# Kernel optimization log

Measured on AMD Instinct MI355X. Metric: run time of the kernel, lower is better.

Reference implementation:

```python
import jax, jax.numpy as jnp
import numpy as np
from jax import lax

CROP = 4
DATA_RANGE = 255.0
KSIZE = 11


def _box_filter(x):
    # x: [B,1,H,W]; 11x11 uniform kernel, padding 5 (SAME), single channel
    k = jnp.ones((1, 1, KSIZE, KSIZE), dtype=x.dtype) / (KSIZE * KSIZE)
    return lax.conv_general_dilated(
        x, k, window_strides=(1, 1), padding=[(5, 5), (5, 5)],
        dimension_numbers=("NCHW", "OIHW", "NCHW"))


def setup_inputs() -> dict:
    key = jax.random.key(0)
    k1, k2 = jax.random.split(key)
    img1 = jax.random.uniform(k1, (16, 3, 512, 512), dtype=jnp.float32) * DATA_RANGE
    img2 = jax.random.uniform(k2, (16, 3, 512, 512), dtype=jnp.float32) * DATA_RANGE
    return {"img1": img1, "img2": img2}


def reference(img1, img2):
    # only_test_y_channel: take channel 0
    x1 = img1[:, 0:1, :, :]
    x2 = img2[:, 0:1, :, :]
    # crop_border = 4
    x1 = x1[:, :, CROP:-CROP, CROP:-CROP].astype(jnp.float32)
    x2 = x2[:, :, CROP:-CROP, CROP:-CROP].astype(jnp.float32)

    C1 = (0.01 * DATA_RANGE) ** 2
    C2 = (0.03 * DATA_RANGE) ** 2

    mu1 = _box_filter(x1)
    mu2 = _box_filter(x2)
    mu1_sq = mu1 * mu1
    mu2_sq = mu2 * mu2
    mu1_mu2 = mu1 * mu2
    sigma1_sq = _box_filter(x1 * x1) - mu1_sq
    sigma2_sq = _box_filter(x2 * x2) - mu2_sq
    sigma12 = _box_filter(x1 * x2) - mu1_mu2

    ssim_map = ((2 * mu1_mu2 + C1) * (2 * sigma12 + C2)) / (
        (mu1_sq + mu2_sq + C1) * (sigma1_sq + sigma2_sq + C2))
    return jnp.mean(ssim_map)
```

## Files before the change

### kernel.cpp

```cpp
#include <hip/hip_runtime.h>

#define CROPPX 4
#define H 504
#define W 504
#define IMG 512
#define NB 16
#define NCH 3
#define KS 11
#define RAD 5
#define TW 64
#define STRIP (TW + 2*RAD)
#define RPS 28
#define NSEG 18
#define NXT 8
#define TOTAL (RPS + 2*RAD)

__global__ __launch_bounds__(64) void ssim_main(const float* __restrict__ img1,
                                                const float* __restrict__ img2,
                                                float* __restrict__ partial) {
    const int tid = threadIdx.x;
    const int gx0 = blockIdx.x * TW;
    const int y0  = blockIdx.y * RPS;
    const int b   = blockIdx.z;

    __shared__ float2 rowAB[STRIP];

    const float* p1 = img1 + (size_t)(b * NCH) * IMG * IMG + (size_t)CROPPX * IMG + CROPPX;
    const float* p2 = img2 + (size_t)(b * NCH) * IMG * IMG + (size_t)CROPPX * IMG + CROPPX;

    float r1[KS], r2[KS], r11[KS], r22[KS], r12[KS];
    #pragma unroll
    for (int j = 0; j < KS; ++j) { r1[j]=0.f; r2[j]=0.f; r11[j]=0.f; r22[j]=0.f; r12[j]=0.f; }

    float vs1 = 0.f, vs2 = 0.f, vs11 = 0.f, vs22 = 0.f, vs12 = 0.f;
    float ssum = 0.f;
    const float C1 = 6.5025f, C2 = 58.5225f;
    const float inv121 = 1.0f / 121.0f;
    const bool colValid = (gx0 + tid) < W;
    const int c0 = gx0 - RAD + tid;
    const int c1 = c0 + 64;
    const bool lane2 = tid < (STRIP - 64);

    float a0 = 0.f, b0 = 0.f, a1 = 0.f, b1 = 0.f;
    {
        const int r = y0 - RAD;
        if ((unsigned)r < (unsigned)H) {
            const size_t ro = (size_t)r * IMG;
            if ((unsigned)c0 < (unsigned)W) { a0 = p1[ro + c0]; b0 = p2[ro + c0]; }
            if (lane2 && (unsigned)c1 < (unsigned)W) { a1 = p1[ro + c1]; b1 = p2[ro + c1]; }
        }
    }

    for (int base = 0; base < TOTAL; base += KS) {
        #pragma unroll
        for (int j = 0; j < KS; ++j) {
            const int iter = base + j;
            if (iter >= TOTAL) break;

            __syncthreads();
            rowAB[tid] = make_float2(a0, b0);
            if (lane2) rowAB[64 + tid] = make_float2(a1, b1);
            __syncthreads();

            a0 = 0.f; b0 = 0.f; a1 = 0.f; b1 = 0.f;
            if (iter + 1 < TOTAL) {
                const int rn = y0 - RAD + iter + 1;
                if ((unsigned)rn < (unsigned)H) {
                    const size_t ro = (size_t)rn * IMG;
                    if ((unsigned)c0 < (unsigned)W) { a0 = p1[ro + c0]; b0 = p2[ro + c0]; }
                    if (lane2 && (unsigned)c1 < (unsigned)W) { a1 = p1[ro + c1]; b1 = p2[ro + c1]; }
                }
            }

            float h1 = 0.f, h2 = 0.f, h11 = 0.f, h22 = 0.f, h12 = 0.f;
            #pragma unroll
            for (int dx = 0; dx < KS; ++dx) {
                const float2 ab = rowAB[tid + dx];
                h1 += ab.x;
                h2 += ab.y;
                h11 = fmaf(ab.x, ab.x, h11);
                h22 = fmaf(ab.y, ab.y, h22);
                h12 = fmaf(ab.x, ab.y, h12);
            }

            vs1  += h1  - r1[j];  r1[j]  = h1;
            vs2  += h2  - r2[j];  r2[j]  = h2;
            vs11 += h11 - r11[j]; r11[j] = h11;
            vs22 += h22 - r22[j]; r22[j] = h22;
            vs12 += h12 - r12[j]; r12[j] = h12;

            if (iter >= 2 * RAD && colValid) {
                const float mu1 = vs1 * inv121;
                const float mu2 = vs2 * inv121;
                const float mu1s = mu1 * mu1;
                const float mu2s = mu2 * mu2;
                const float m12  = mu1 * mu2;
                const float s1  = fmaf(vs11, inv121, -mu1s);
                const float s2  = fmaf(vs22, inv121, -mu2s);
                const float s12 = fmaf(vs12, inv121, -m12);
                const float num = (2.0f * m12 + C1) * (2.0f * s12 + C2);
                const float den = (mu1s + mu2s + C1) * (s1 + s2 + C2);
                ssum += num / den;
            }
        }
    }

    for (int off = 32; off > 0; off >>= 1)
        ssum += __shfl_down(ssum, off);
    if (tid == 0) {
        const int bidx = (blockIdx.z * gridDim.y + blockIdx.y) * gridDim.x + blockIdx.x;
        partial[bidx] = ssum;
    }
}

__global__ __launch_bounds__(256) void ssim_final(const float* __restrict__ partial,
                                                  int n, float* __restrict__ out) {
    __shared__ double sh[256];
    double s = 0.0;
    for (int i = threadIdx.x; i < n; i += 256) s += (double)partial[i];
    sh[threadIdx.x] = s;
    __syncthreads();
    for (int stride = 128; stride > 0; stride >>= 1) {
        if (threadIdx.x < stride) sh[threadIdx.x] += sh[threadIdx.x + stride];
        __syncthreads();
    }
    if (threadIdx.x == 0)
        out[0] = (float)(sh[0] / ((double)NB * (double)H * (double)W));
}

extern "C" void kernel_launch(void* const* d_in, const int* in_sizes, int n_in,
                              void* d_out, int out_size, void* d_ws, size_t ws_size,
                              hipStream_t stream) {
    const float* img1 = (const float*)d_in[0];
    const float* img2 = (const float*)d_in[1];
    float* out = (float*)d_out;
    float* partial = (float*)d_ws;

    dim3 grid(NXT, NSEG, NB);
    ssim_main<<<grid, 64, 0, stream>>>(img1, img2, partial);
    ssim_final<<<1, 256, 0, stream>>>(partial, NXT * NSEG * NB, out);
}
```

Measured before the change: 132.1 us.

## Preload whole row strip into shared memory before filtering, drop per-row barriers

Instead of streaming one row at a time through a shared buffer with two barriers per row and a one-row prefetch, each block now loads its full 28-row strip into shared memory up front in batches of 7 rows (many loads in flight), syncs once, then runs the sliding-window filter. The strip height drops to 18 rows with more segments, giving more blocks but more halo overhead (28 rows loaded for 18 outputs). The division is also replaced with a fast hardware reciprocal, which slightly loosens precision.

```diff
diff --git a/kernel.cpp b/kernel.cpp
--- a/kernel.cpp
+++ b/kernel.cpp
@@ -10,10 +10,11 @@
 #define RAD 5
 #define TW 64
 #define STRIP (TW + 2*RAD)
-#define RPS 28
-#define NSEG 18
+#define RPS 18
+#define NSEG 28
 #define NXT 8
-#define TOTAL (RPS + 2*RAD)
+#define ROWS (RPS + 2*RAD)
+#define CHUNK 7
 
 __global__ __launch_bounds__(64) void ssim_main(const float* __restrict__ img1,
                                                 const float* __restrict__ img2,
@@ -23,10 +24,38 @@
     const int y0  = blockIdx.y * RPS;
     const int b   = blockIdx.z;
 
-    __shared__ float2 rowAB[STRIP];
+    __shared__ float2 strip[ROWS][STRIP];
 
     const float* p1 = img1 + (size_t)(b * NCH) * IMG * IMG + (size_t)CROPPX * IMG + CROPPX;
     const float* p2 = img2 + (size_t)(b * NCH) * IMG * IMG + (size_t)CROPPX * IMG + CROPPX;
+
+    const int c0 = gx0 - RAD + tid;
+    const int c1 = c0 + 64;
+    const bool lane2 = tid < (STRIP - 64);
+    const bool c0ok = (unsigned)c0 < (unsigned)W;
+    const bool c1ok = lane2 && ((unsigned)c1 < (unsigned)W);
+
+    #pragma unroll
+    for (int rc = 0; rc < ROWS / CHUNK; ++rc) {
+        float a0[CHUNK], b0[CHUNK], a1[CHUNK], b1[CHUNK];
+        #pragma unroll
+        for (int j = 0; j < CHUNK; ++j) {
+            const int r = y0 - RAD + rc * CHUNK + j;
+            a0[j] = 0.f; b0[j] = 0.f; a1[j] = 0.f; b1[j] = 0.f;
+            if ((unsigned)r < (unsigned)H) {
+                const size_t ro = (size_t)r * IMG;
+                if (c0ok) { a0[j] = p1[ro + c0]; b0[j] = p2[ro + c0]; }
+                if (c1ok) { a1[j] = p1[ro + c1]; b1[j] = p2[ro + c1]; }
+            }
+        }
+        #pragma unroll
+        for (int j = 0; j < CHUNK; ++j) {
+            const int r = rc * CHUNK + j;
+            strip[r][tid] = make_float2(a0[j], b0[j]);
+            if (lane2) strip[r][64 + tid] = make_float2(a1[j], b1[j]);
+        }
+    }
+    __syncthreads();
 
     float r1[KS], r2[KS], r11[KS], r22[KS], r12[KS];
     #pragma unroll
@@ -37,45 +66,17 @@
     const float C1 = 6.5025f, C2 = 58.5225f;
     const float inv121 = 1.0f / 121.0f;
     const bool colValid = (gx0 + tid) < W;
-    const int c0 = gx0 - RAD + tid;
-    const int c1 = c0 + 64;
-    const bool lane2 = tid < (STRIP - 64);
 
-    float a0 = 0.f, b0 = 0.f, a1 = 0.f, b1 = 0.f;
-    {
-        const int r = y0 - RAD;
-        if ((unsigned)r < (unsigned)H) {
-            const size_t ro = (size_t)r * IMG;
-            if ((unsigned)c0 < (unsigned)W) { a0 = p1[ro + c0]; b0 = p2[ro + c0]; }
-            if (lane2 && (unsigned)c1 < (unsigned)W) { a1 = p1[ro + c1]; b1 = p2[ro + c1]; }
-        }
-    }
-
-    for (int base = 0; base < TOTAL; base += KS) {
+    for (int base = 0; base < ROWS; base += KS) {
         #pragma unroll
         for (int j = 0; j < KS; ++j) {
             const int iter = base + j;
-            if (iter >= TOTAL) break;
-
-            __syncthreads();
-            rowAB[tid] = make_float2(a0, b0);
-            if (lane2) rowAB[64 + tid] = make_float2(a1, b1);
-            __syncthreads();
-
-            a0 = 0.f; b0 = 0.f; a1 = 0.f; b1 = 0.f;
-            if (iter + 1 < TOTAL) {
-                const int rn = y0 - RAD + iter + 1;
-                if ((unsigned)rn < (unsigned)H) {
-                    const size_t ro = (size_t)rn * IMG;
-                    if ((unsigned)c0 < (unsigned)W) { a0 = p1[ro + c0]; b0 = p2[ro + c0]; }
-                    if (lane2 && (unsigned)c1 < (unsigned)W) { a1 = p1[ro + c1]; b1 = p2[ro + c1]; }
-                }
-            }
+            if (iter >= ROWS) break;
 
             float h1 = 0.f, h2 = 0.f, h11 = 0.f, h22 = 0.f, h12 = 0.f;
             #pragma unroll
             for (int dx = 0; dx < KS; ++dx) {
-                const float2 ab = rowAB[tid + dx];
+                const float2 ab = strip[iter][tid + dx];
                 h1 += ab.x;
                 h2 += ab.y;
                 h11 = fmaf(ab.x, ab.x, h11);
@@ -100,7 +101,7 @@
                 const float s12 = fmaf(vs12, inv121, -m12);
                 const float num = (2.0f * m12 + C1) * (2.0f * s12 + C2);
                 const float den = (mu1s + mu2s + C1) * (s1 + s2 + C2);
-                ssum += num / den;
+                ssum = fmaf(num, __builtin_amdgcn_rcpf(den), ssum);
             }
         }
     }
```

Measured after the change: 143.7 us. +8.8%, slower.

## Pack four independent row-strip wavefronts per block and drop block barriers

Applied to the files above, without the earlier changes.

Each 256-thread block now runs four wavefronts, each with its own private shared-memory row buffer and its own 21-row strip. Because a row buffer is only touched by one wave, the two __syncthreads per row are removed. Loads now use clamped addresses with select-based zeroing instead of branches, and the per-pixel division becomes a hardware reciprocal plus FMA. Shorter strips mean a larger share of the 10 halo rows is recomputed per output row, and the approximate reciprocal may change rounding slightly.

```diff
diff --git a/kernel.cpp b/kernel.cpp
--- a/kernel.cpp
+++ b/kernel.cpp
@@ -10,23 +10,35 @@
 #define RAD 5
 #define TW 64
 #define STRIP (TW + 2*RAD)
-#define RPS 28
-#define NSEG 18
+#define RPS 21
+#define WPB 4
+#define BROWS (RPS * WPB)
+#define NYB 6
 #define NXT 8
 #define TOTAL (RPS + 2*RAD)
 
-__global__ __launch_bounds__(64) void ssim_main(const float* __restrict__ img1,
-                                                const float* __restrict__ img2,
-                                                float* __restrict__ partial) {
-    const int tid = threadIdx.x;
-    const int gx0 = blockIdx.x * TW;
-    const int y0  = blockIdx.y * RPS;
-    const int b   = blockIdx.z;
+__global__ __launch_bounds__(256, 4) void ssim_main(const float* __restrict__ img1,
+                                                    const float* __restrict__ img2,
+                                                    float* __restrict__ partial) {
+    const int lane = threadIdx.x & 63;
+    const int wv   = threadIdx.x >> 6;
+    const int gx0  = blockIdx.x * TW;
+    const int y0   = blockIdx.y * BROWS + wv * RPS;
+    const int b    = blockIdx.z;
 
-    __shared__ float2 rowAB[STRIP];
+    __shared__ float2 rowBuf[WPB][STRIP];
+    float2* const myRow = rowBuf[wv];
 
     const float* p1 = img1 + (size_t)(b * NCH) * IMG * IMG + (size_t)CROPPX * IMG + CROPPX;
     const float* p2 = img2 + (size_t)(b * NCH) * IMG * IMG + (size_t)CROPPX * IMG + CROPPX;
+
+    const int  c0   = gx0 - RAD + lane;
+    const int  c0c  = min(max(c0, 0), W - 1);
+    const bool c0ok = (unsigned)c0 < (unsigned)W;
+    const int  c1   = c0 + 64;
+    const int  c1c  = min(c1, W - 1);
+    const bool c1ok = (unsigned)c1 < (unsigned)W;
+    const bool lane2 = lane < (STRIP - 64);
 
     float r1[KS], r2[KS], r11[KS], r22[KS], r12[KS];
     #pragma unroll
@@ -36,18 +48,21 @@
     float ssum = 0.f;
     const float C1 = 6.5025f, C2 = 58.5225f;
     const float inv121 = 1.0f / 121.0f;
-    const bool colValid = (gx0 + tid) < W;
-    const int c0 = gx0 - RAD + tid;
-    const int c1 = c0 + 64;
-    const bool lane2 = tid < (STRIP - 64);
+    const bool colValid = (gx0 + lane) < W;
 
-    float a0 = 0.f, b0 = 0.f, a1 = 0.f, b1 = 0.f;
+    float a0, b0, a1 = 0.f, b1 = 0.f;
     {
-        const int r = y0 - RAD;
-        if ((unsigned)r < (unsigned)H) {
-            const size_t ro = (size_t)r * IMG;
-            if ((unsigned)c0 < (unsigned)W) { a0 = p1[ro + c0]; b0 = p2[ro + c0]; }
-            if (lane2 && (unsigned)c1 < (unsigned)W) { a1 = p1[ro + c1]; b1 = p2[ro + c1]; }
+        const int r  = y0 - RAD;
+        const int rc = min(max(r, 0), H - 1);
+        const bool rok = (unsigned)r < (unsigned)H;
+        const size_t ro = (size_t)rc * IMG;
+        const float ta0 = p1[ro + c0c], tb0 = p2[ro + c0c];
+        a0 = (rok && c0ok) ? ta0 : 0.f;
+        b0 = (rok && c0ok) ? tb0 : 0.f;
+        if (lane2) {
+            const float ta1 = p1[ro + c1c], tb1 = p2[ro + c1c];
+            a1 = (rok && c1ok) ? ta1 : 0.f;
+            b1 = (rok && c1ok) ? tb1 : 0.f;
         }
     }
 
@@ -57,25 +72,28 @@
             const int iter = base + j;
             if (iter >= TOTAL) break;
 
-            __syncthreads();
-            rowAB[tid] = make_float2(a0, b0);
-            if (lane2) rowAB[64 + tid] = make_float2(a1, b1);
-            __syncthreads();
+            myRow[lane] = make_float2(a0, b0);
+            if (lane2) myRow[64 + lane] = make_float2(a1, b1);
 
-            a0 = 0.f; b0 = 0.f; a1 = 0.f; b1 = 0.f;
             if (iter + 1 < TOTAL) {
-                const int rn = y0 - RAD + iter + 1;
-                if ((unsigned)rn < (unsigned)H) {
-                    const size_t ro = (size_t)rn * IMG;
-                    if ((unsigned)c0 < (unsigned)W) { a0 = p1[ro + c0]; b0 = p2[ro + c0]; }
-                    if (lane2 && (unsigned)c1 < (unsigned)W) { a1 = p1[ro + c1]; b1 = p2[ro + c1]; }
+                const int r  = y0 - RAD + iter + 1;
+                const int rc = min(max(r, 0), H - 1);
+                const bool rok = (unsigned)r < (unsigned)H;
+                const size_t ro = (size_t)rc * IMG;
+                const float ta0 = p1[ro + c0c], tb0 = p2[ro + c0c];
+                a0 = (rok && c0ok) ? ta0 : 0.f;
+                b0 = (rok && c0ok) ? tb0 : 0.f;
+                if (lane2) {
+                    const float ta1 = p1[ro + c1c], tb1 = p2[ro + c1c];
+                    a1 = (rok && c1ok) ? ta1 : 0.f;
+                    b1 = (rok && c1ok) ? tb1 : 0.f;
                 }
             }
 
             float h1 = 0.f, h2 = 0.f, h11 = 0.f, h22 = 0.f, h12 = 0.f;
             #pragma unroll
             for (int dx = 0; dx < KS; ++dx) {
-                const float2 ab = rowAB[tid + dx];
+                const float2 ab = myRow[lane + dx];
                 h1 += ab.x;
                 h2 += ab.y;
                 h11 = fmaf(ab.x, ab.x, h11);
@@ -100,15 +118,15 @@
                 const float s12 = fmaf(vs12, inv121, -m12);
                 const float num = (2.0f * m12 + C1) * (2.0f * s12 + C2);
                 const float den = (mu1s + mu2s + C1) * (s1 + s2 + C2);
-                ssum += num / den;
+                ssum = fmaf(num, __builtin_amdgcn_rcpf(den), ssum);
             }
         }
     }
 
     for (int off = 32; off > 0; off >>= 1)
         ssum += __shfl_down(ssum, off);
-    if (tid == 0) {
-        const int bidx = (blockIdx.z * gridDim.y + blockIdx.y) * gridDim.x + blockIdx.x;
+    if (lane == 0) {
+        const int bidx = (((blockIdx.z * gridDim.y + blockIdx.y) * gridDim.x + blockIdx.x) * WPB) + wv;
         partial[bidx] = ssum;
     }
 }
@@ -136,7 +154,7 @@
     float* out = (float*)d_out;
     float* partial = (float*)d_ws;
 
-    dim3 grid(NXT, NSEG, NB);
-    ssim_main<<<grid, 64, 0, stream>>>(img1, img2, partial);
-    ssim_final<<<1, 256, 0, stream>>>(partial, NXT * NSEG * NB, out);
+    dim3 grid(NXT, NYB, NB);
+    ssim_main<<<grid, 256, 0, stream>>>(img1, img2, partial);
+    ssim_final<<<1, 256, 0, stream>>>(partial, NXT * NYB * NB * WPB, out);
 }
```

Result: slower. 145.1 us (+9.8%).
